# Kernel optimization log

Measured on AMD Instinct MI355X. Metric: run time of the kernel, lower is better.

Reference implementation:

```python
import jax, jax.numpy as jnp
import numpy as np

N_HEADS = 16
D_HEAD = 64
D_MODEL = 1024


def apply_rotary_emb(t, cos, sin):
    # t: (B, H, T, D), cos/sin: (T, D//2) -> half-split rotation
    d2 = t.shape[-1] // 2
    t1, t2 = t[..., :d2], t[..., d2:]
    cos = cos[None, None, :, :]
    sin = sin[None, None, :, :]
    return jnp.concatenate([t1 * cos - t2 * sin, t1 * sin + t2 * cos], axis=-1)


def setup_inputs() -> dict:
    key = jax.random.key(0)
    ks = jax.random.split(key, 8)
    B, T = 2, 2048
    x = jax.random.normal(ks[0], (B, T, D_MODEL), dtype=jnp.float32)
    # rotary cache built from standard inv-freq schedule
    inv_freq = 1.0 / (10000.0 ** (jnp.arange(0, D_HEAD, 2, dtype=jnp.float32) / D_HEAD))
    ang = jnp.arange(T, dtype=jnp.float32)[:, None] * inv_freq[None, :]  # (T, D/2)
    cos, sin = jnp.cos(ang), jnp.sin(ang)
    s = 1.0 / np.sqrt(D_MODEL)
    W_q = jax.random.normal(ks[1], (D_MODEL, N_HEADS * D_HEAD), dtype=jnp.float32) * s
    W_k = jax.random.normal(ks[2], (D_MODEL, N_HEADS * D_HEAD), dtype=jnp.float32) * s
    W_v = jax.random.normal(ks[3], (D_MODEL, N_HEADS * D_HEAD), dtype=jnp.float32) * s
    W_out = jax.random.normal(ks[4], (N_HEADS * D_HEAD, D_MODEL), dtype=jnp.float32) * s
    return {"x": x, "cos": cos, "sin": sin, "W_q": W_q, "W_k": W_k, "W_v": W_v, "W_out": W_out}


def reference(x, cos, sin, W_q, W_k, W_v, W_out):
    B, T, _ = x.shape
    def split_heads(t):
        return t.reshape(B, T, N_HEADS, D_HEAD).transpose(0, 2, 1, 3)  # (B,H,T,D)
    q = split_heads(x @ W_q)
    k = split_heads(x @ W_k)
    v = split_heads(x @ W_v)
    q = apply_rotary_emb(q, cos, sin)
    k = apply_rotary_emb(k, cos, sin)
    scores = jnp.einsum('bhqd,bhkd->bhqk', q, k) / np.sqrt(D_HEAD).astype(np.float32)
    causal = jnp.triu(jnp.ones((T, T), dtype=bool), k=1)
    scores = jnp.where(causal[None, None], -jnp.inf, scores)
    attn = jax.nn.softmax(scores, axis=-1)
    z = jnp.einsum('bhqk,bhkd->bhqd', attn, v)
    z = z.transpose(0, 2, 1, 3).reshape(B, T, N_HEADS * D_HEAD)
    return z @ W_out
```

## Files before the change

### kernel.cpp

```cpp
#include <hip/hip_runtime.h>

typedef __attribute__((ext_vector_type(4))) float f32x4;
typedef __attribute__((ext_vector_type(8))) short short8;
typedef __attribute__((ext_vector_type(8))) unsigned short u16x8;
typedef __attribute__((ext_vector_type(4))) unsigned short u16x4;
typedef __attribute__((ext_vector_type(2))) unsigned int u32x2;

#define D_MODEL 1024
#define NHEADS 16
#define T_SEQ 2048
#define M_TOT 4096

__device__ __forceinline__ unsigned short f2bf(float f) {
    union { float f; unsigned int u; } v; v.f = f;
    return (unsigned short)((v.u + 0x7fffu + ((v.u >> 16) & 1u)) >> 16);
}
__device__ __forceinline__ float bf2f(unsigned short b) {
    union { unsigned int u; float f; } v; v.u = ((unsigned int)b) << 16;
    return v.f;
}
__device__ __forceinline__ unsigned int cvtpk_bf16(float lo, float hi) {
    unsigned int r;
    asm("v_cvt_pk_bf16_f32 %0, %1, %2" : "=v"(r) : "v"(lo), "v"(hi));
    return r;
}

#define GLD0(dst, addr) \
    asm volatile("global_load_dwordx4 %0, %1, off" : "=v"(dst) : "v"(addr) : "memory")
#define WAITV0() do { asm volatile("s_waitcnt vmcnt(0)" ::: "memory"); \
                      __builtin_amdgcn_sched_barrier(0); } while (0)
#define LBAR() do { asm volatile("s_waitcnt lgkmcnt(0)" ::: "memory"); \
                    __builtin_amdgcn_s_barrier(); \
                    __builtin_amdgcn_sched_barrier(0); } while (0)

#define GLDS16(gp, lp) \
    __builtin_amdgcn_global_load_lds((const __attribute__((address_space(1))) void*)(gp), \
                                     (__attribute__((address_space(3))) void*)(lp), 16, 0, 0)

__global__ __launch_bounds__(256) void prep_kernel(const float* __restrict__ X,
                                                   unsigned short* __restrict__ Xb,
                                                   const float* __restrict__ W0,
                                                   const float* __restrict__ W1,
                                                   const float* __restrict__ W2,
                                                   const float* __restrict__ W3,
                                                   unsigned short* __restrict__ Wt0) {
    __shared__ float tile[64][65];
    const int z = blockIdx.z;
    if (z >= 4) {
        const int blk = (z - 4) * 256 + blockIdx.y * 16 + blockIdx.x;
        const int i = (blk * 256 + threadIdx.x) * 4;
        const float4 v = *(const float4*)(X + i);
        u16x4 r;
        r.x = f2bf(v.x); r.y = f2bf(v.y); r.z = f2bf(v.z); r.w = f2bf(v.w);
        *(u16x4*)(Xb + i) = r;
        return;
    }
    const float* W = (z == 0) ? W0 : (z == 1) ? W1 : (z == 2) ? W2 : W3;
    unsigned short* Wt = Wt0 + (size_t)z * D_MODEL * D_MODEL;
    const int n0 = blockIdx.x * 64, k0 = blockIdx.y * 64;
    for (int i = threadIdx.x; i < 4096; i += 256) {
        const int r = i >> 6, c = i & 63;
        tile[r][c] = W[(size_t)(k0 + r) * D_MODEL + n0 + c];
    }
    __syncthreads();
    for (int i = threadIdx.x; i < 4096; i += 256) {
        const int r = i >> 6, c = i & 63;
        Wt[(size_t)(n0 + r) * D_MODEL + k0 + c] = f2bf(tile[c][r]);
    }
}

#define TN_G 128
#define BK_G 32

template<int MI, int OUTMODE>
__global__ __launch_bounds__(256) void gemm_kernel(
    const unsigned short* __restrict__ A,
    const unsigned short* __restrict__ Bt0,
    void* __restrict__ Cout0,
    const float* __restrict__ cosp,
    const float* __restrict__ sinp,
    float* __restrict__ Kmax)
{
    constexpr int TMc = MI * 32;
    constexpr int NCHA = TMc / 16;
    __shared__ unsigned short sA[TMc * 32];
    __shared__ unsigned short sB[TN_G * 32];

    const int tid = threadIdx.x;
    const int wid = tid >> 6;
    const int lane = tid & 63;
    const int quad = lane >> 4;
    const int l16 = lane & 15;
    const int wm = wid >> 1, wn = wid & 1;
    const int m0 = blockIdx.x * TMc, n0 = blockIdx.y * TN_G;
    const int z = blockIdx.z;
    const unsigned short* Bt = Bt0 + (size_t)z * D_MODEL * D_MODEL;
    const int srowL = lane >> 2;
    const int scolL = (lane & 3) * 8;

    f32x4 acc[MI][4] = {};

    for (int k0 = 0; k0 < D_MODEL; k0 += BK_G) {
        #pragma unroll
        for (int ch = wid; ch < NCHA + 8; ch += 4) {
            if (ch < NCHA) {
                GLDS16(A + (size_t)(m0 + ch * 16 + srowL) * D_MODEL + k0 + scolL,
                       &sA[ch * 512]);
            } else {
                GLDS16(Bt + (size_t)(n0 + (ch - NCHA) * 16 + srowL) * D_MODEL + k0 + scolL,
                       &sB[(ch - NCHA) * 512]);
            }
        }
        __syncthreads();

        short8 af[MI], bf[4];
        #pragma unroll
        for (int i = 0; i < MI; ++i)
            af[i] = *(const short8*)&sA[(wm * (MI * 16) + i * 16 + l16) * 32 + quad * 8];
        #pragma unroll
        for (int i = 0; i < 4; ++i)
            bf[i] = *(const short8*)&sB[(wn * 64 + i * 16 + l16) * 32 + quad * 8];
        #pragma unroll
        for (int mi = 0; mi < MI; ++mi)
            #pragma unroll
            for (int ni = 0; ni < 4; ++ni)
                acc[mi][ni] = __builtin_amdgcn_mfma_f32_16x16x32_bf16(af[mi], bf[ni], acc[mi][ni], 0, 0, 0);
        __syncthreads();
    }

    if constexpr (OUTMODE == 0) {
        float* C = (float*)Cout0;
        #pragma unroll
        for (int mi = 0; mi < MI; ++mi) {
            const int mb = m0 + wm * (MI * 16) + mi * 16 + quad * 4;
            #pragma unroll
            for (int ni = 0; ni < 4; ++ni) {
                const int n = n0 + wn * 64 + ni * 16 + l16;
                #pragma unroll
                for (int r = 0; r < 4; ++r)
                    C[(size_t)(mb + r) * D_MODEL + n] = acc[mi][ni][r];
            }
        }
    } else {
        unsigned short* O = (unsigned short*)Cout0 + (size_t)z * M_TOT * D_MODEL;
        const int h = (n0 + wn * 64) >> 6;
        if (z == 2) {
            #pragma unroll
            for (int mi = 0; mi < MI; ++mi) {
                const int mb = m0 + wm * (MI * 16) + mi * 16 + quad * 4;
                const int b = mb >> 11, t = mb & (T_SEQ - 1);
                #pragma unroll
                for (int ni = 0; ni < 4; ++ni) {
                    const int d = ni * 16 + l16;
                    u16x4 pk;
                    #pragma unroll
                    for (int r = 0; r < 4; ++r) pk[r] = f2bf(acc[mi][ni][r]);
                    *(u16x4*)(O + ((size_t)(b * NHEADS + h) * 64 + d) * T_SEQ + t) = pk;
                }
            }
        } else {
            if (z == 1) {
                float mx = 0.f;
                #pragma unroll
                for (int mi = 0; mi < MI; ++mi)
                    #pragma unroll
                    for (int r = 0; r < 4; ++r) {
                        float s = 0.f;
                        #pragma unroll
                        for (int ni = 0; ni < 4; ++ni) s += acc[mi][ni][r] * acc[mi][ni][r];
                        s += __shfl_xor(s, 1); s += __shfl_xor(s, 2);
                        s += __shfl_xor(s, 4); s += __shfl_xor(s, 8);
                        mx = fmaxf(mx, s);
                    }
                mx = fmaxf(mx, __shfl_xor(mx, 16));
                mx = fmaxf(mx, __shfl_xor(mx, 32));
                if (lane == 0) {
                    const int b = m0 >> 11;
                    const int slot = ((m0 >> 7) & 15) * 2 + wm;
                    Kmax[(size_t)(b * NHEADS + h) * 32 + slot] = __builtin_sqrtf(mx);
                }
            }
            const float qs = (z == 0) ? 0.125f : 1.0f;
            #pragma unroll
            for (int mi = 0; mi < MI; ++mi) {
                #pragma unroll
                for (int r = 0; r < 4; ++r) {
                    const int m = m0 + wm * (MI * 16) + mi * 16 + quad * 4 + r;
                    const int b = m >> 11, t = m & (T_SEQ - 1);
                    const size_t rowoff = ((size_t)(b * NHEADS + h) * T_SEQ + t) * 64;
                    #pragma unroll
                    for (int ni = 0; ni < 2; ++ni) {
                        const int d = ni * 16 + l16;
                        const float c = cosp[t * 32 + d], s = sinp[t * 32 + d];
                        const float x1 = acc[mi][ni][r], x2 = acc[mi][ni + 2][r];
                        O[rowoff + d]      = f2bf((x1 * c - x2 * s) * qs);
                        O[rowoff + d + 32] = f2bf((x1 * s + x2 * c) * qs);
                    }
                }
            }
        }
    }
}

#define LOG2E 1.44269504f

struct AttnSmem {
    union {
        unsigned short kv[2][4][4096];
        float comb[4][64][34];
    } u;
    unsigned short P[8][16 * 64];
};

__global__ __launch_bounds__(512, 2) void attn_kernel(
    const unsigned short* __restrict__ Q,
    const unsigned short* __restrict__ Kg,
    const unsigned short* __restrict__ Vt,
    const float* __restrict__ Kseg,
    unsigned short* __restrict__ Z)
{
    __shared__ AttnSmem sm;

    const int tid = threadIdx.x;
    const int wid = tid >> 6;
    const int w4 = wid & 3;
    const int half = wid >> 2;
    const int lane = tid & 63;
    const int quad = lane >> 4;
    const int l16 = lane & 15;
    const int srow = tid >> 3;
    const int sslot = tid & 7;
    const int wslot = sslot ^ (srow & 7);
    const int sxK = (quad ^ (l16 & 7)) << 3;
    const int ph8 = (l16 & 7) << 3;

    const int flat = blockIdx.x + 16 * blockIdx.y;
    const int xcd = flat & 7, idx = flat >> 3;
    const int bh = xcd * 4 + (idx & 3);
    const int x = idx >> 2;

    const int qA = x, qB = 31 - x;
    const int jend = 31 - x;

    const unsigned short* Qp = Q + (size_t)bh * T_SEQ * 64;
    const unsigned short* Kp = Kg + (size_t)bh * T_SEQ * 64;
    const unsigned short* Vp = Vt + (size_t)bh * 64 * T_SEQ;

    short8 aqA[2], aqB[2];
    {
        const unsigned short* qr = Qp + (size_t)(qA * 64 + w4 * 16 + l16) * 64 + quad * 8;
        aqA[0] = *(const short8*)(qr);
        aqA[1] = *(const short8*)(qr + 32);
        qr = Qp + (size_t)(qB * 64 + w4 * 16 + l16) * 64 + quad * 8;
        aqB[0] = *(const short8*)(qr);
        aqB[1] = *(const short8*)(qr + 32);
    }

    float kmx = 0.f;
    #pragma unroll
    for (int i = 0; i < 32; ++i) kmx = fmaxf(kmx, Kseg[bh * 32 + i]);

    float mQA, mQB;
    {
        float nqA = 0.f, nqB = 0.f;
        #pragma unroll
        for (int i = 0; i < 2; ++i)
            #pragma unroll
            for (int e = 0; e < 8; ++e) {
                const float fa = bf2f((unsigned short)aqA[i][e]);
                const float fb = bf2f((unsigned short)aqB[i][e]);
                nqA += fa * fa; nqB += fb * fb;
            }
        nqA += __shfl_xor(nqA, 16); nqA += __shfl_xor(nqA, 32);
        nqB += __shfl_xor(nqB, 16); nqB += __shfl_xor(nqB, 32);
        mQA = __builtin_sqrtf(nqA) * kmx * LOG2E;
        mQB = __builtin_sqrtf(nqB) * kmx * LOG2E;
    }

    auto tile_pack = [&](f32x4 (&s)[4], float mQ, float& lsum, bool msk,
                         unsigned short* Pw) {
        if (msk) {
            #pragma unroll
            for (int nt = 0; nt < 4; ++nt)
                #pragma unroll
                for (int r = 0; r < 4; ++r)
                    if (nt * 16 + quad * 4 + r > w4 * 16 + l16) s[nt][r] = -1e30f;
        }
        #pragma unroll
        for (int nt = 0; nt < 4; ++nt) {
            const float p0 = __builtin_exp2f(s[nt][0] * LOG2E - mQ);
            const float p1 = __builtin_exp2f(s[nt][1] * LOG2E - mQ);
            const float p2 = __builtin_exp2f(s[nt][2] * LOG2E - mQ);
            const float p3 = __builtin_exp2f(s[nt][3] * LOG2E - mQ);
            lsum += (p0 + p1) + (p2 + p3);
            const unsigned int w0 = cvtpk_bf16(p0, p1);
            const unsigned int w1 = cvtpk_bf16(p2, p3);
            *(u32x2*)&Pw[l16 * 64 + ((nt * 16 + quad * 4) ^ ph8)] = (u32x2){w0, w1};
        }
    };

    f32x4 oA[4] = {}, oB[4] = {};
    float lA = 0.f, lB = 0.f;
    unsigned short* Pw = &sm.P[wid][0];

    short8 stg[4];
    auto ISSUE = [&](int t) {
        const int j0 = 2 * t, j1 = j0 + 1;
        GLD0(stg[0], Kp + (size_t)j0 * 4096 + tid * 8);
        GLD0(stg[1], Vp + (size_t)srow * 2048 + j0 * 64 + sslot * 8);
        GLD0(stg[2], Kp + (size_t)j1 * 4096 + tid * 8);
        GLD0(stg[3], Vp + (size_t)srow * 2048 + j1 * 64 + sslot * 8);
    };
    auto WRITE = [&](int b) {
        const int dst = srow * 64 + (wslot << 3);
        *(short8*)&sm.u.kv[b][0][dst] = stg[0];
        *(short8*)&sm.u.kv[b][1][dst] = stg[1];
        *(short8*)&sm.u.kv[b][2][dst] = stg[2];
        *(short8*)&sm.u.kv[b][3][dst] = stg[3];
    };

    auto COMPUTE = [&](int j, int b) {
        if (j > jend) return;
        const bool doA = (j <= x);
        const unsigned short* sKb = &sm.u.kv[b][half * 2][0];
        const unsigned short* sVb = &sm.u.kv[b][half * 2 + 1][0];
        f32x4 sA[4] = {}, sB[4] = {};
        __builtin_amdgcn_s_setprio(1);
        #pragma unroll
        for (int nt = 0; nt < 4; ++nt) {
            const int rb = (nt * 16 + l16) * 64;
            const short8 k0 = *(const short8*)&sKb[rb + sxK];
            const short8 k1 = *(const short8*)&sKb[rb + (sxK ^ 32)];
            if (doA) {
                sA[nt] = __builtin_amdgcn_mfma_f32_16x16x32_bf16(k0, aqA[0], sA[nt], 0, 0, 0);
                sA[nt] = __builtin_amdgcn_mfma_f32_16x16x32_bf16(k1, aqA[1], sA[nt], 0, 0, 0);
            }
            sB[nt] = __builtin_amdgcn_mfma_f32_16x16x32_bf16(k0, aqB[0], sB[nt], 0, 0, 0);
            sB[nt] = __builtin_amdgcn_mfma_f32_16x16x32_bf16(k1, aqB[1], sB[nt], 0, 0, 0);
        }
        __builtin_amdgcn_s_setprio(0);
        short8 pfA0 = {}, pfA1 = {};
        if (doA) {
            tile_pack(sA, mQA, lA, j == x, Pw);
            asm volatile("s_waitcnt lgkmcnt(0)" ::: "memory");
            pfA0 = *(const short8*)&Pw[l16 * 64 + ((quad * 8) ^ ph8)];
            pfA1 = *(const short8*)&Pw[l16 * 64 + ((32 + quad * 8) ^ ph8)];
        }
        tile_pack(sB, mQB, lB, j == jend, Pw);
        asm volatile("s_waitcnt lgkmcnt(0)" ::: "memory");
        const short8 pfB0 = *(const short8*)&Pw[l16 * 64 + ((quad * 8) ^ ph8)];
        const short8 pfB1 = *(const short8*)&Pw[l16 * 64 + ((32 + quad * 8) ^ ph8)];
        __builtin_amdgcn_s_setprio(1);
        #pragma unroll
        for (int dt = 0; dt < 4; ++dt) {
            const int rb = (dt * 16 + l16) * 64;
            const short8 v0 = *(const short8*)&sVb[rb + sxK];
            const short8 v1 = *(const short8*)&sVb[rb + (sxK ^ 32)];
            if (doA) {
                oA[dt] = __builtin_amdgcn_mfma_f32_16x16x32_bf16(pfA0, v0, oA[dt], 0, 0, 0);
                oA[dt] = __builtin_amdgcn_mfma_f32_16x16x32_bf16(pfA1, v1, oA[dt], 0, 0, 0);
            }
            oB[dt] = __builtin_amdgcn_mfma_f32_16x16x32_bf16(pfB0, v0, oB[dt], 0, 0, 0);
            oB[dt] = __builtin_amdgcn_mfma_f32_16x16x32_bf16(pfB1, v1, oB[dt], 0, 0, 0);
        }
        __builtin_amdgcn_s_setprio(0);
    };

    const int nr = (jend >> 1) + 1;
    ISSUE(0);
    WAITV0();
    WRITE(0);
    LBAR();
    for (int t = 0; t < nr; ++t) {
        const bool more = (t + 1 < nr);
        if (more) ISSUE(t + 1);
        COMPUTE(2 * t + half, t & 1);
        if (more) {
            WAITV0();
            WRITE((t + 1) & 1);
        }
        LBAR();
    }

    lA += __shfl_xor(lA, 16); lA += __shfl_xor(lA, 32);
    lB += __shfl_xor(lB, 16); lB += __shfl_xor(lB, 32);

    __syncthreads();
    if (half) {
        float* cb = &sm.u.comb[w4][lane][0];
        #pragma unroll
        for (int dt = 0; dt < 4; ++dt)
            #pragma unroll
            for (int r = 0; r < 4; ++r) {
                cb[dt * 4 + r]      = oA[dt][r];
                cb[16 + dt * 4 + r] = oB[dt][r];
            }
        cb[32] = lA; cb[33] = lB;
    }
    __syncthreads();
    if (half) return;

    {
        const float* cb = &sm.u.comb[w4][lane][0];
        #pragma unroll
        for (int dt = 0; dt < 4; ++dt)
            #pragma unroll
            for (int r = 0; r < 4; ++r) {
                oA[dt][r] += cb[dt * 4 + r];
                oB[dt][r] += cb[16 + dt * 4 + r];
            }
        lA += cb[32]; lB += cb[33];
    }

    const float iA = 1.f / lA, iB = 1.f / lB;
    float irA[4], irB[4];
    #pragma unroll
    for (int r = 0; r < 4; ++r) {
        const int src = (lane & 48) | (quad * 4 + r);
        irA[r] = __shfl(iA, src);
        irB[r] = __shfl(iB, src);
    }

    const int h = bh & 15, b = bh >> 4;
    #pragma unroll
    for (int dt = 0; dt < 4; ++dt)
        #pragma unroll
        for (int r = 0; r < 4; ++r) {
            const int rowA = qA * 64 + w4 * 16 + quad * 4 + r;
            const int rowB = qB * 64 + w4 * 16 + quad * 4 + r;
            const int col = h * 64 + dt * 16 + l16;
            Z[((size_t)b * T_SEQ + rowA) * D_MODEL + col] = f2bf(oA[dt][r] * irA[r]);
            Z[((size_t)b * T_SEQ + rowB) * D_MODEL + col] = f2bf(oB[dt][r] * irB[r]);
        }
}

extern "C" void kernel_launch(void* const* d_in, const int* in_sizes, int n_in,
                              void* d_out, int out_size, void* d_ws, size_t ws_size,
                              hipStream_t stream) {
    const float* x    = (const float*)d_in[0];
    const float* cosp = (const float*)d_in[1];
    const float* sinp = (const float*)d_in[2];
    const float* Wq   = (const float*)d_in[3];
    const float* Wk   = (const float*)d_in[4];
    const float* Wv   = (const float*)d_in[5];
    const float* Wo   = (const float*)d_in[6];

    char* w = (char*)d_ws;
    unsigned short* xb  = (unsigned short*)w; w += (size_t)M_TOT * D_MODEL * 2;
    unsigned short* wt  = (unsigned short*)w; w += (size_t)4 * D_MODEL * D_MODEL * 2;
    unsigned short* Qb  = (unsigned short*)w; w += (size_t)M_TOT * D_MODEL * 2;
    unsigned short* Kb  = (unsigned short*)w; w += (size_t)M_TOT * D_MODEL * 2;
    unsigned short* Vtb = (unsigned short*)w; w += (size_t)M_TOT * D_MODEL * 2;
    unsigned short* Zb  = (unsigned short*)w; w += (size_t)M_TOT * D_MODEL * 2;
    float*          Ks  = (float*)w;          w += 32 * 32 * sizeof(float);

    prep_kernel<<<dim3(16, 16, 20), 256, 0, stream>>>(x, xb, Wq, Wk, Wv, Wo, wt);

    gemm_kernel<4, 1><<<dim3(M_TOT / 128, D_MODEL / 128, 3), 256, 0, stream>>>(
        xb, wt, (void*)Qb, cosp, sinp, Ks);

    attn_kernel<<<dim3(16, 32), 512, 0, stream>>>(Qb, Kb, Vtb, Ks, Zb);

    gemm_kernel<2, 0><<<dim3(M_TOT / 64, D_MODEL / 128, 1), 256, 0, stream>>>(
        Zb, wt + (size_t)3 * D_MODEL * D_MODEL, d_out, nullptr, nullptr, nullptr);
}
```

Before: 212.2 us.

## Double-buffer GEMM LDS tiles with BK=64 and XOR-swizzled layout

Rewrites the GEMM main loop so the next K-tile is staged into a second LDS buffer with direct global-to-LDS loads while the current tile is computed. This removes one barrier per step and overlaps memory with MFMA work. K depth per tile doubles to 64, and an XOR swizzle on the column chunk avoids LDS bank conflicts. The output projection also moves to 128-row tiles. The cost is double the LDS footprint and fewer blocks for the final GEMM, which may lower occupancy.

Measured after the change: 205.5 us. -3.2%, faster.

```diff
diff --git a/kernel.cpp b/kernel.cpp
--- a/kernel.cpp
+++ b/kernel.cpp
@@ -70,7 +70,7 @@
 }
 
 #define TN_G 128
-#define BK_G 32
+#define BK_G 64
 
 template<int MI, int OUTMODE>
 __global__ __launch_bounds__(256) void gemm_kernel(
@@ -82,9 +82,10 @@
     float* __restrict__ Kmax)
 {
     constexpr int TMc = MI * 32;
-    constexpr int NCHA = TMc / 16;
-    __shared__ unsigned short sA[TMc * 32];
-    __shared__ unsigned short sB[TN_G * 32];
+    constexpr int NCHA = TMc / 8;
+    constexpr int NCHB = TN_G / 8;
+    __shared__ unsigned short sA[2][TMc * 64];
+    __shared__ unsigned short sB[2][TN_G * 64];
 
     const int tid = threadIdx.x;
     const int wid = tid >> 6;
@@ -95,37 +96,50 @@
     const int m0 = blockIdx.x * TMc, n0 = blockIdx.y * TN_G;
     const int z = blockIdx.z;
     const unsigned short* Bt = Bt0 + (size_t)z * D_MODEL * D_MODEL;
-    const int srowL = lane >> 2;
-    const int scolL = (lane & 3) * 8;
+    const int r8 = lane >> 3;
+    const int c8 = lane & 7;
+    const int cswz = (c8 ^ r8) * 8;
+    const int rx = l16 & 7;
 
     f32x4 acc[MI][4] = {};
 
-    for (int k0 = 0; k0 < D_MODEL; k0 += BK_G) {
-        #pragma unroll
-        for (int ch = wid; ch < NCHA + 8; ch += 4) {
-            if (ch < NCHA) {
-                GLDS16(A + (size_t)(m0 + ch * 16 + srowL) * D_MODEL + k0 + scolL,
-                       &sA[ch * 512]);
-            } else {
-                GLDS16(Bt + (size_t)(n0 + (ch - NCHA) * 16 + srowL) * D_MODEL + k0 + scolL,
-                       &sB[(ch - NCHA) * 512]);
-            }
-        }
-        __syncthreads();
-
-        short8 af[MI], bf[4];
-        #pragma unroll
-        for (int i = 0; i < MI; ++i)
-            af[i] = *(const short8*)&sA[(wm * (MI * 16) + i * 16 + l16) * 32 + quad * 8];
-        #pragma unroll
-        for (int i = 0; i < 4; ++i)
-            bf[i] = *(const short8*)&sB[(wn * 64 + i * 16 + l16) * 32 + quad * 8];
-        #pragma unroll
-        for (int mi = 0; mi < MI; ++mi)
-            #pragma unroll
-            for (int ni = 0; ni < 4; ++ni)
-                acc[mi][ni] = __builtin_amdgcn_mfma_f32_16x16x32_bf16(af[mi], bf[ni], acc[mi][ni], 0, 0, 0);
-        __syncthreads();
+    auto STAGE = [&](int b, int k0) {
+        for (int ch = wid; ch < NCHA + NCHB; ch += 4) {
+            if (ch < NCHA)
+                GLDS16(A + (size_t)(m0 + ch * 8 + r8) * D_MODEL + k0 + cswz,
+                       &sA[b][ch * 512]);
+            else
+                GLDS16(Bt + (size_t)(n0 + (ch - NCHA) * 8 + r8) * D_MODEL + k0 + cswz,
+                       &sB[b][(ch - NCHA) * 512]);
+        }
+    };
+    auto COMPUTE = [&](int b) {
+        #pragma unroll
+        for (int ks = 0; ks < 2; ++ks) {
+            const int sx = ((ks * 4 + quad) ^ rx) * 8;
+            short8 af[MI], bf[4];
+            #pragma unroll
+            for (int i = 0; i < MI; ++i)
+                af[i] = *(const short8*)&sA[b][(wm * (MI * 16) + i * 16 + l16) * 64 + sx];
+            #pragma unroll
+            for (int i = 0; i < 4; ++i)
+                bf[i] = *(const short8*)&sB[b][(wn * 64 + i * 16 + l16) * 64 + sx];
+            #pragma unroll
+            for (int mi = 0; mi < MI; ++mi)
+                #pragma unroll
+                for (int ni = 0; ni < 4; ++ni)
+                    acc[mi][ni] = __builtin_amdgcn_mfma_f32_16x16x32_bf16(af[mi], bf[ni], acc[mi][ni], 0, 0, 0);
+        }
+    };
+
+    STAGE(0, 0);
+    WAITV0();
+    LBAR();
+    for (int kk = 0; kk < D_MODEL / BK_G; ++kk) {
+        if (kk + 1 < D_MODEL / BK_G) STAGE((kk + 1) & 1, (kk + 1) * BK_G);
+        COMPUTE(kk & 1);
+        WAITV0();
+        LBAR();
     }
 
     if constexpr (OUTMODE == 0) {
@@ -461,6 +475,6 @@
 
     attn_kernel<<<dim3(16, 32), 512, 0, stream>>>(Qb, Kb, Vtb, Ks, Zb);
 
-    gemm_kernel<2, 0><<<dim3(M_TOT / 64, D_MODEL / 128, 1), 256, 0, stream>>>(
+    gemm_kernel<4, 0><<<dim3(M_TOT / 128, D_MODEL / 128, 1), 256, 0, stream>>>(
         Zb, wt + (size_t)3 * D_MODEL * D_MODEL, d_out, nullptr, nullptr, nullptr);
 }
```
